# Optimization experiments

Hardware: AMD Instinct MI355X
Metric: run time of the kernel (lower is better)

The kernel has to match this reference:

```python
import jax, jax.numpy as jnp
import numpy as np
from jax import lax

B, S, D = 2, 4096, 1024
E, H, K = 8, 2816, 2  # hidden_dim 4096 -> int(2*4096/3)=2730 -> round up to multiple_of 256 -> 2816


def setup_inputs() -> dict:
    key = jax.random.key(0)
    ks = jax.random.split(key, 5)
    scale = 0.02
    return {
        "x": jax.random.normal(ks[0], (B, S, D), dtype=jnp.float32),
        "router_w": jax.random.normal(ks[1], (E, D), dtype=jnp.float32) * scale,
        "w1": jax.random.normal(ks[2], (E, D, H), dtype=jnp.float32) * scale,
        "w2": jax.random.normal(ks[3], (E, H, D), dtype=jnp.float32) * scale,
        "w3": jax.random.normal(ks[4], (E, D, H), dtype=jnp.float32) * scale,
        "top_k": K,
    }


def reference(x, router_w, w1, w2, w3, top_k):
    b, s, d = x.shape
    e = router_w.shape[0]
    xf = x.reshape(-1, d)                                # [T, D]
    logits = xf @ router_w.T                             # [T, E]
    vals, idx = lax.top_k(logits, top_k)                 # [T, K]
    rw = jax.nn.softmax(vals.astype(jnp.float32), axis=-1).astype(x.dtype)  # [T, K]
    # combine[t, e] = routing weight of expert e for token t (0 if not selected)
    combine = jnp.sum(jax.nn.one_hot(idx, e, dtype=x.dtype) * rw[..., None], axis=1)  # [T, E]

    def body(acc, ew):
        w1e, w2e, w3e, ce = ew                           # [D,H], [H,D], [D,H], [T]
        h = jax.nn.silu(xf @ w1e) * (xf @ w3e)           # SwiGLU FFN, [T, H]
        return acc + (h @ w2e) * ce[:, None], None

    out, _ = lax.scan(body, jnp.zeros_like(xf), (w1, w2, w3, combine.T))
    return out.reshape(b, s, d)
```

## Files before the change

kernel.cpp:

```cpp
#include <hip/hip_runtime.h>
#include <stdint.h>

#define T_TOK 8192
#define DIM   1024
#define NE    8
#define NH    2816
#define NROWS (T_TOK*2)

typedef __attribute__((ext_vector_type(8))) __bf16 bf16x8;
typedef __attribute__((ext_vector_type(4))) float  f32x4;

typedef __attribute__((address_space(1))) const unsigned int g_as1;
typedef __attribute__((address_space(3))) unsigned int l_as3;
#define GLL(g, l) __builtin_amdgcn_global_load_lds((g_as1*)(g), (l_as3*)(l), 16, 0, 0)

__device__ __forceinline__ unsigned short f2bf(float f){
  union { float f; uint32_t u; } v; v.f = f;
  uint32_t r = (v.u + 0x7FFFu + ((v.u >> 16) & 1u)) >> 16;
  return (unsigned short)r;
}


__global__ void init_k(int* counts, int* cursor){
  int i = threadIdx.x;
  if (i < NE){ counts[i] = 0; cursor[i] = 0; }
}

__global__ void zero_out_k(float4* __restrict__ out){
  int i = blockIdx.x*blockDim.x + threadIdx.x;
  const int n4 = T_TOK*DIM/4;
  const float4 z = make_float4(0.f,0.f,0.f,0.f);
  for (; i < n4; i += gridDim.x*blockDim.x) out[i] = z;
}

__global__ void cvt_k(const float* __restrict__ x, unsigned short* __restrict__ xbf){
  int i = blockIdx.x*blockDim.x + threadIdx.x;
  const int total = T_TOK*DIM/8;
  for (; i < total; i += gridDim.x*blockDim.x){
    const float4 a = *(const float4*)(x + (size_t)i*8);
    const float4 b = *(const float4*)(x + (size_t)i*8 + 4);
    ushort4 lo = make_ushort4(f2bf(a.x), f2bf(a.y), f2bf(a.z), f2bf(a.w));
    ushort4 hi = make_ushort4(f2bf(b.x), f2bf(b.y), f2bf(b.z), f2bf(b.w));
    *(ushort4*)(xbf + (size_t)i*8)     = lo;
    *(ushort4*)(xbf + (size_t)i*8 + 4) = hi;
  }
}

__global__ __launch_bounds__(256) void transp_k(const float* __restrict__ in,
    unsigned short* __restrict__ outp, int R, int C)
{
  __shared__ unsigned short Tl[64*68];
  const int r0 = blockIdx.x*64, c0 = blockIdx.y*64;
  const size_t mbase = (size_t)blockIdx.z * (size_t)R * (size_t)C;
  const float* ip = in + mbase;
  unsigned short* op = outp + mbase;
  const int t = threadIdx.x;
  #pragma unroll
  for (int i=0;i<4;i++){
    const int r  = (t>>4) + i*16;
    const int cq = t & 15;
    const float4 v = *(const float4*)(ip + (size_t)(r0+r)*C + c0 + cq*4);
    Tl[(cq*4+0)*68 + r] = f2bf(v.x);
    Tl[(cq*4+1)*68 + r] = f2bf(v.y);
    Tl[(cq*4+2)*68 + r] = f2bf(v.z);
    Tl[(cq*4+3)*68 + r] = f2bf(v.w);
  }
  __syncthreads();
  #pragma unroll
  for (int i=0;i<4;i++){
    const int idx = i*1024 + t*4;
    const int c = idx>>6, r = idx&63;
    const ushort4 v = *(const ushort4*)&Tl[c*68 + r];
    *(ushort4*)(op + (size_t)(c0+c)*R + r0 + r) = v;
  }
}

__global__ __launch_bounds__(256) void transp2_k(const float* __restrict__ w1,
    const float* __restrict__ w3, unsigned short* __restrict__ w1t,
    unsigned short* __restrict__ w3t)
{
  __shared__ unsigned short Tl[64*68];
  const int r0 = blockIdx.x*64, c0 = blockIdx.y*64;
  const int z = blockIdx.z;
  const size_t mbase = (size_t)(z & (NE-1)) * (size_t)DIM * (size_t)NH;
  const float* ip = (z < NE ? w1 : w3) + mbase;
  unsigned short* op = (z < NE ? w1t : w3t) + mbase;
  const int t = threadIdx.x;
  #pragma unroll
  for (int i=0;i<4;i++){
    const int r  = (t>>4) + i*16;
    const int cq = t & 15;
    const float4 v = *(const float4*)(ip + (size_t)(r0+r)*NH + c0 + cq*4);
    Tl[(cq*4+0)*68 + r] = f2bf(v.x);
    Tl[(cq*4+1)*68 + r] = f2bf(v.y);
    Tl[(cq*4+2)*68 + r] = f2bf(v.z);
    Tl[(cq*4+3)*68 + r] = f2bf(v.w);
  }
  __syncthreads();
  #pragma unroll
  for (int i=0;i<4;i++){
    const int idx = i*1024 + t*4;
    const int c = idx>>6, r = idx&63;
    const ushort4 v = *(const ushort4*)&Tl[c*68 + r];
    *(ushort4*)(op + (size_t)(c0+c)*DIM + r0 + r) = v;
  }
}


__global__ void router_k(const float* __restrict__ x, const float* __restrict__ rw,
                         int* __restrict__ topk_e, float* __restrict__ topk_w,
                         int* __restrict__ counts){
  const int t = blockIdx.x;
  const int l = threadIdx.x;
  const float* xr = x + (size_t)t * DIM;
  float acc[NE];
  #pragma unroll
  for (int e=0;e<NE;e++) acc[e] = 0.f;
  #pragma unroll
  for (int i=0;i<DIM/64;i++){
    float xv = xr[l + 64*i];
    #pragma unroll
    for (int e=0;e<NE;e++) acc[e] += xv * rw[e*DIM + l + 64*i];
  }
  #pragma unroll
  for (int e=0;e<NE;e++){
    float v = acc[e];
    #pragma unroll
    for (int off=32; off; off>>=1) v += __shfl_xor(v, off);
    acc[e] = v;
  }
  if (l == 0){
    int e0 = 0; float v0 = acc[0];
    #pragma unroll
    for (int e=1;e<NE;e++) if (acc[e] > v0){ v0 = acc[e]; e0 = e; }
    int e1 = -1; float v1 = -1e30f;
    #pragma unroll
    for (int e=0;e<NE;e++) if (e != e0 && acc[e] > v1){ v1 = acc[e]; e1 = e; }
    float ex = __expf(v1 - v0);
    float s  = 1.f + ex;
    topk_e[t*2]   = e0;  topk_e[t*2+1] = e1;
    topk_w[t*2]   = 1.f/s; topk_w[t*2+1] = ex/s;
    atomicAdd(&counts[e0], 1);
    atomicAdd(&counts[e1], 1);
  }
}

__global__ void prefix_k(const int* __restrict__ counts, int* __restrict__ offs){
  if (threadIdx.x == 0 && blockIdx.x == 0){
    int s = 0;
    for (int e=0;e<NE;e++){ offs[e] = s; s += counts[e]; }
  }
}

__global__ void scatter_k(const int* __restrict__ topk_e, const float* __restrict__ topk_w,
                          const int* __restrict__ offs, int* __restrict__ cursor,
                          int* __restrict__ row_tok, float* __restrict__ row_w){
  int t = blockIdx.x*blockDim.x + threadIdx.x;
  if (t >= T_TOK) return;
  #pragma unroll
  for (int k=0;k<2;k++){
    int e = topk_e[t*2+k];
    int p = atomicAdd(&cursor[e], 1);
    int flat = offs[e] + p;
    row_tok[flat] = t;
    row_w[flat]   = topk_w[t*2+k];
  }
}


__global__ __launch_bounds__(512,2) void gemm1_p(
    const unsigned short* __restrict__ xbf,
    const unsigned short* __restrict__ w1t, const unsigned short* __restrict__ w3t,
    unsigned short* __restrict__ hbuf,
    const int* __restrict__ row_tok,
    const int* __restrict__ counts, const int* __restrict__ offs)
{
  __shared__ unsigned short As [3][128*32];
  __shared__ unsigned short B1s[3][128*32];
  __shared__ unsigned short B3s[3][128*32];

  const int i   = blockIdx.y*64 + blockIdx.x;
  const int lid = (i & 7)*1408 + (i >> 3);
  const int e   = lid / 1408;
  const int rem = lid - e*1408;
  const int h0  = (rem >> 6) * 128;
  const int rb  = rem & 63;

  const int cnt = counts[e];
  const int row0 = rb * 128;
  if (row0 >= cnt) return;
  const int nv   = min(128, cnt - row0);
  const int base = offs[e] + row0;
  const int NK   = DIM/32;

  const int t = threadIdx.x;
  const int r_loc = t >> 2, sct = t & 3;
  const int csw = (sct ^ ((r_loc >> 1) & 3)) * 8;
  const int tok = row_tok[base + min(r_loc, nv-1)];
  const unsigned short* aS  = xbf + (size_t)tok*DIM + csw;
  const unsigned short* b1S = w1t + ((size_t)(e*NH + h0) + r_loc)*DIM + csw;
  const unsigned short* b3S = w3t + ((size_t)(e*NH + h0) + r_loc)*DIM + csw;
  const int lo = t*16;

  const int wid = t >> 6, l = t & 63;
  const int wr = wid >> 2, wc = wid & 3;
  const int lr = l & 15,  lk = l >> 4;
  const int rc = (lk ^ ((lr >> 1) & 3)) * 8;

  f32x4 acc1[4][2], acc3[4][2];
  #pragma unroll
  for (int m=0;m<4;m++)
    #pragma unroll
    for (int n=0;n<2;n++){ acc1[m][n] = (f32x4)0.f; acc3[m][n] = (f32x4)0.f; }

  GLL(aS,      (char*)As[0]+lo); GLL(b1S,      (char*)B1s[0]+lo); GLL(b3S,      (char*)B3s[0]+lo);
  GLL(aS+32,   (char*)As[1]+lo); GLL(b1S+32,   (char*)B1s[1]+lo); GLL(b3S+32,   (char*)B3s[1]+lo);

  for (int kt=0; kt<NK; ++kt){
    if (kt < NK-1) asm volatile("s_waitcnt vmcnt(3)" ::: "memory");
    else           asm volatile("s_waitcnt vmcnt(0)" ::: "memory");
    __builtin_amdgcn_s_barrier();

    if (kt+2 < NK){
      const int kA = (kt+2)*32;
      char* ad  = (char*)As [(kt+2)%3];
      char* b1d = (char*)B1s[(kt+2)%3];
      char* b3d = (char*)B3s[(kt+2)%3];
      GLL(aS+kA, ad+lo); GLL(b1S+kA, b1d+lo); GLL(b3S+kA, b3d+lo);
    }

    const unsigned short* Ab  = As [kt%3];
    const unsigned short* B1b = B1s[kt%3];
    const unsigned short* B3b = B3s[kt%3];

    bf16x8 a[4], b1[2], b3[2];
    #pragma unroll
    for (int m=0;m<4;m++) a[m] = *(const bf16x8*)&Ab[(wr*64 + m*16 + lr)*32 + rc];
    #pragma unroll
    for (int n=0;n<2;n++){
      b1[n] = *(const bf16x8*)&B1b[(wc*32 + n*16 + lr)*32 + rc];
      b3[n] = *(const bf16x8*)&B3b[(wc*32 + n*16 + lr)*32 + rc];
    }
    __builtin_amdgcn_s_setprio(1);
    #pragma unroll
    for (int m=0;m<4;m++)
      #pragma unroll
      for (int n=0;n<2;n++){
        acc1[m][n] = __builtin_amdgcn_mfma_f32_16x16x32_bf16(a[m], b1[n], acc1[m][n], 0,0,0);
        acc3[m][n] = __builtin_amdgcn_mfma_f32_16x16x32_bf16(a[m], b3[n], acc3[m][n], 0,0,0);
      }
    __builtin_amdgcn_s_setprio(0);
  }

  #pragma unroll
  for (int m=0;m<4;m++){
    #pragma unroll
    for (int i2=0;i2<4;i2++){
      const int r = wr*64 + m*16 + lk*4 + i2;
      if (r < nv){
        const size_t rowbase = (size_t)(base + r) * NH;
        #pragma unroll
        for (int n=0;n<2;n++){
          float z  = acc1[m][n][i2];
          float p3 = acc3[m][n][i2];
          float hv = (z / (1.f + __expf(-z))) * p3;
          hbuf[rowbase + h0 + wc*32 + n*16 + lr] = f2bf(hv);
        }
      }
    }
  }
}

__global__ __launch_bounds__(512,2) void gemm2_p(
    const unsigned short* __restrict__ hbuf,
    const unsigned short* __restrict__ w2t,
    float* __restrict__ out,
    const int* __restrict__ row_tok, const float* __restrict__ row_w,
    const int* __restrict__ counts, const int* __restrict__ offs)
{
  __shared__ unsigned short As[3][128*32];
  __shared__ unsigned short Bs[3][128*32];

  const int i   = blockIdx.y*64 + blockIdx.x;
  const int lid = (i & 7)*512 + (i >> 3);
  const int e   = lid >> 9;
  const int rem = lid & 511;
  const int d0  = (rem >> 6) * 128;
  const int rb  = rem & 63;

  const int cnt = counts[e];
  const int row0 = rb * 128;
  if (row0 >= cnt) return;
  const int nv   = min(128, cnt - row0);
  const int base = offs[e] + row0;
  const int NK   = NH/32;

  const int t = threadIdx.x;
  const int r_loc = t >> 2, sct = t & 3;
  const int csw = (sct ^ ((r_loc >> 1) & 3)) * 8;
  const unsigned short* aS = hbuf + (size_t)(base + min(r_loc, nv-1))*NH + csw;
  const unsigned short* bS = w2t + ((size_t)(e*DIM + d0) + r_loc)*NH + csw;
  const int lo = t*16;

  const int wid = t >> 6, l = t & 63;
  const int wr = wid >> 2, wc = wid & 3;
  const int lr = l & 15,  lk = l >> 4;
  const int rc = (lk ^ ((lr >> 1) & 3)) * 8;

  f32x4 acc[4][2];
  #pragma unroll
  for (int m=0;m<4;m++)
    #pragma unroll
    for (int n=0;n<2;n++) acc[m][n] = (f32x4)0.f;

  GLL(aS,    (char*)As[0]+lo); GLL(bS,    (char*)Bs[0]+lo);
  GLL(aS+32, (char*)As[1]+lo); GLL(bS+32, (char*)Bs[1]+lo);

  for (int kt=0; kt<NK; ++kt){
    if (kt < NK-1) asm volatile("s_waitcnt vmcnt(2)" ::: "memory");
    else           asm volatile("s_waitcnt vmcnt(0)" ::: "memory");
    __builtin_amdgcn_s_barrier();

    if (kt+2 < NK){
      const int kA = (kt+2)*32;
      char* ad = (char*)As[(kt+2)%3];
      char* bd = (char*)Bs[(kt+2)%3];
      GLL(aS+kA, ad+lo); GLL(bS+kA, bd+lo);
    }

    const unsigned short* Ab = As[kt%3];
    const unsigned short* Bb = Bs[kt%3];

    bf16x8 a[4], b[2];
    #pragma unroll
    for (int m=0;m<4;m++) a[m] = *(const bf16x8*)&Ab[(wr*64 + m*16 + lr)*32 + rc];
    #pragma unroll
    for (int n=0;n<2;n++)  b[n] = *(const bf16x8*)&Bb[(wc*32 + n*16 + lr)*32 + rc];
    __builtin_amdgcn_s_setprio(1);
    #pragma unroll
    for (int m=0;m<4;m++)
      #pragma unroll
      for (int n=0;n<2;n++)
        acc[m][n] = __builtin_amdgcn_mfma_f32_16x16x32_bf16(a[m], b[n], acc[m][n], 0,0,0);
    __builtin_amdgcn_s_setprio(0);
  }

  #pragma unroll
  for (int m=0;m<4;m++){
    #pragma unroll
    for (int i2=0;i2<4;i2++){
      const int r = wr*64 + m*16 + lk*4 + i2;
      if (r < nv){
        const int flat = base + r;
        const int tok  = row_tok[flat];
        const float wgt = row_w[flat];
        float* orow = out + (size_t)tok * DIM + d0 + wc*32;
        #pragma unroll
        for (int n=0;n<2;n++)
          atomicAdd(&orow[n*16 + lr], acc[m][n][i2] * wgt);
      }
    }
  }
}


__global__ __launch_bounds__(256) void gemm1_k(
    const unsigned short* __restrict__ xbf,
    const float* __restrict__ w1, const float* __restrict__ w3,
    unsigned short* __restrict__ hbuf,
    const int* __restrict__ row_tok,
    const int* __restrict__ counts, const int* __restrict__ offs)
{
  __shared__ unsigned short Al [128*32];
  __shared__ unsigned short B1l[128*32];
  __shared__ unsigned short B3l[128*32];
  const int e   = blockIdx.y >> 6;
  const int rb  = blockIdx.y & 63;
  const int cnt = counts[e];
  const int row0 = rb * 128;
  if (row0 >= cnt) return;
  const int nv   = min(128, cnt - row0);
  const int base = offs[e] + row0;
  const int h0   = blockIdx.x * 128;
  const int t  = threadIdx.x;
  const int ar0 = t >> 2;
  const int ac  = t & 3;
  const int tok0 = row_tok[base + min(ar0,      nv-1)];
  const int tok1 = row_tok[base + min(ar0 + 64, nv-1)];
  const size_t asrc0 = (size_t)tok0 * DIM + ac*8;
  const size_t asrc1 = (size_t)tok1 * DIM + ac*8;
  const int dg = t >> 5;
  const int hq = t & 31;
  const float* w1p = w1 + (size_t)e * DIM * NH + (size_t)(h0 + hq*4);
  const float* w3p = w3 + (size_t)e * DIM * NH + (size_t)(h0 + hq*4);
  const int wid = t >> 6, l = t & 63;
  const int wr = wid >> 1, wc = wid & 1;
  const int lr = l & 15,  lk = l >> 4;
  f32x4 acc1[4][4], acc3[4][4];
  #pragma unroll
  for (int m=0;m<4;m++)
    #pragma unroll
    for (int n=0;n<4;n++){ acc1[m][n] = (f32x4)0.f; acc3[m][n] = (f32x4)0.f; }
  for (int kk=0; kk<DIM/32; ++kk){
    const int k0 = kk*32;
    __syncthreads();
    *(uint4*)&Al[ar0*32 + ac*8]      = *(const uint4*)(xbf + asrc0 + k0);
    *(uint4*)&Al[(ar0+64)*32 + ac*8] = *(const uint4*)(xbf + asrc1 + k0);
    {
      const float4 f0 = *(const float4*)(w1p + (size_t)(k0 + dg*4 + 0)*NH);
      const float4 f1 = *(const float4*)(w1p + (size_t)(k0 + dg*4 + 1)*NH);
      const float4 f2 = *(const float4*)(w1p + (size_t)(k0 + dg*4 + 2)*NH);
      const float4 f3 = *(const float4*)(w1p + (size_t)(k0 + dg*4 + 3)*NH);
      const float* p0=(const float*)&f0; const float* p1=(const float*)&f1;
      const float* p2=(const float*)&f2; const float* p3=(const float*)&f3;
      #pragma unroll
      for (int j=0;j<4;j++){
        ushort4 pk = make_ushort4(f2bf(p0[j]), f2bf(p1[j]), f2bf(p2[j]), f2bf(p3[j]));
        *(ushort4*)&B1l[(hq*4+j)*32 + dg*4] = pk;
      }
      const float4 g0 = *(const float4*)(w3p + (size_t)(k0 + dg*4 + 0)*NH);
      const float4 g1 = *(const float4*)(w3p + (size_t)(k0 + dg*4 + 1)*NH);
      const float4 g2 = *(const float4*)(w3p + (size_t)(k0 + dg*4 + 2)*NH);
      const float4 g3 = *(const float4*)(w3p + (size_t)(k0 + dg*4 + 3)*NH);
      const float* q0=(const float*)&g0; const float* q1=(const float*)&g1;
      const float* q2=(const float*)&g2; const float* q3=(const float*)&g3;
      #pragma unroll
      for (int j=0;j<4;j++){
        ushort4 pk = make_ushort4(f2bf(q0[j]), f2bf(q1[j]), f2bf(q2[j]), f2bf(q3[j]));
        *(ushort4*)&B3l[(hq*4+j)*32 + dg*4] = pk;
      }
    }
    __syncthreads();
    bf16x8 a[4], b1[4], b3[4];
    #pragma unroll
    for (int m=0;m<4;m++) a[m] = *(const bf16x8*)&Al[(wr*64 + m*16 + lr)*32 + lk*8];
    #pragma unroll
    for (int n=0;n<4;n++){
      b1[n] = *(const bf16x8*)&B1l[(wc*64 + n*16 + lr)*32 + lk*8];
      b3[n] = *(const bf16x8*)&B3l[(wc*64 + n*16 + lr)*32 + lk*8];
    }
    #pragma unroll
    for (int m=0;m<4;m++)
      #pragma unroll
      for (int n=0;n<4;n++){
        acc1[m][n] = __builtin_amdgcn_mfma_f32_16x16x32_bf16(a[m], b1[n], acc1[m][n], 0,0,0);
        acc3[m][n] = __builtin_amdgcn_mfma_f32_16x16x32_bf16(a[m], b3[n], acc3[m][n], 0,0,0);
      }
  }
  #pragma unroll
  for (int m=0;m<4;m++){
    #pragma unroll
    for (int i=0;i<4;i++){
      const int r = wr*64 + m*16 + lk*4 + i;
      if (r < nv){
        const size_t rowbase = (size_t)(base + r) * NH;
        #pragma unroll
        for (int n=0;n<4;n++){
          float z  = acc1[m][n][i];
          float p3 = acc3[m][n][i];
          float hv = (z / (1.f + __expf(-z))) * p3;
          hbuf[rowbase + h0 + wc*64 + n*16 + lr] = f2bf(hv);
        }
      }
    }
  }
}

__global__ __launch_bounds__(256) void gemm2_k(
    const unsigned short* __restrict__ hbuf,
    const float* __restrict__ w2,
    float* __restrict__ out,
    const int* __restrict__ row_tok, const float* __restrict__ row_w,
    const int* __restrict__ counts, const int* __restrict__ offs)
{
  __shared__ unsigned short Al[128*32];
  __shared__ unsigned short Bl[128*32];
  const int e   = blockIdx.y >> 6;
  const int rb  = blockIdx.y & 63;
  const int cnt = counts[e];
  const int row0 = rb * 128;
  if (row0 >= cnt) return;
  const int nv   = min(128, cnt - row0);
  const int base = offs[e] + row0;
  const int d0   = blockIdx.x * 128;
  const int t  = threadIdx.x;
  const int ar0 = t >> 2;
  const int ac  = t & 3;
  const size_t asrc0 = (size_t)(base + min(ar0,      nv-1)) * NH + ac*8;
  const size_t asrc1 = (size_t)(base + min(ar0 + 64, nv-1)) * NH + ac*8;
  const int dg = t >> 5;
  const int hq = t & 31;
  const float* w2p = w2 + (size_t)e * NH * DIM + (size_t)(d0 + hq*4);
  const int wid = t >> 6, l = t & 63;
  const int wr = wid >> 1, wc = wid & 1;
  const int lr = l & 15,  lk = l >> 4;
  f32x4 acc[4][4];
  #pragma unroll
  for (int m=0;m<4;m++)
    #pragma unroll
    for (int n=0;n<4;n++) acc[m][n] = (f32x4)0.f;
  for (int kk=0; kk<NH/32; ++kk){
    const int k0 = kk*32;
    __syncthreads();
    *(uint4*)&Al[ar0*32 + ac*8]      = *(const uint4*)(hbuf + asrc0 + k0);
    *(uint4*)&Al[(ar0+64)*32 + ac*8] = *(const uint4*)(hbuf + asrc1 + k0);
    {
      const float4 f0 = *(const float4*)(w2p + (size_t)(k0 + dg*4 + 0)*DIM);
      const float4 f1 = *(const float4*)(w2p + (size_t)(k0 + dg*4 + 1)*DIM);
      const float4 f2 = *(const float4*)(w2p + (size_t)(k0 + dg*4 + 2)*DIM);
      const float4 f3 = *(const float4*)(w2p + (size_t)(k0 + dg*4 + 3)*DIM);
      const float* p0=(const float*)&f0; const float* p1=(const float*)&f1;
      const float* p2=(const float*)&f2; const float* p3=(const float*)&f3;
      #pragma unroll
      for (int j=0;j<4;j++){
        ushort4 pk = make_ushort4(f2bf(p0[j]), f2bf(p1[j]), f2bf(p2[j]), f2bf(p3[j]));
        *(ushort4*)&Bl[(hq*4+j)*32 + dg*4] = pk;
      }
    }
    __syncthreads();
    bf16x8 a[4], b[4];
    #pragma unroll
    for (int m=0;m<4;m++) a[m] = *(const bf16x8*)&Al[(wr*64 + m*16 + lr)*32 + lk*8];
    #pragma unroll
    for (int n=0;n<4;n++)  b[n] = *(const bf16x8*)&Bl[(wc*64 + n*16 + lr)*32 + lk*8];
    #pragma unroll
    for (int m=0;m<4;m++)
      #pragma unroll
      for (int n=0;n<4;n++)
        acc[m][n] = __builtin_amdgcn_mfma_f32_16x16x32_bf16(a[m], b[n], acc[m][n], 0,0,0);
  }
  #pragma unroll
  for (int m=0;m<4;m++){
    #pragma unroll
    for (int i=0;i<4;i++){
      const int r = wr*64 + m*16 + lk*4 + i;
      if (r < nv){
        const int flat = base + r;
        const int tok  = row_tok[flat];
        const float wgt = row_w[flat];
        float* orow = out + (size_t)tok * DIM + d0 + wc*64;
        #pragma unroll
        for (int n=0;n<4;n++)
          atomicAdd(&orow[n*16 + lr], acc[m][n][i] * wgt);
      }
    }
  }
}


extern "C" void kernel_launch(void* const* d_in, const int* in_sizes, int n_in,
                              void* d_out, int out_size, void* d_ws, size_t ws_size,
                              hipStream_t stream) {
  (void)in_sizes; (void)n_in; (void)out_size;
  const float* x   = (const float*)d_in[0];
  const float* rw  = (const float*)d_in[1];
  const float* w1  = (const float*)d_in[2];
  const float* w2  = (const float*)d_in[3];
  const float* w3  = (const float*)d_in[4];
  float* out = (float*)d_out;
  char* ws = (char*)d_ws;

  const size_t SZ_XBF  = (size_t)T_TOK*DIM*2;
  const size_t SZ_HBUF = (size_t)NROWS*NH*2;
  const size_t SZ_WT   = (size_t)NE*NH*DIM*2;
  const size_t SZ_SMALL = (size_t)NROWS*4*2 + (size_t)T_TOK*2*4*2 + 3*64*4 + 4096;
  const size_t NEED_FAST = SZ_XBF + SZ_HBUF + 2*SZ_WT + SZ_SMALL;

  if (ws_size >= NEED_FAST) {
    size_t off = 0;
    unsigned short* xbf  = (unsigned short*)(ws + off); off += SZ_XBF;
    unsigned short* hbuf = (unsigned short*)(ws + off); off += SZ_HBUF;
    unsigned short* w1t  = (unsigned short*)(ws + off); off += SZ_WT;
    unsigned short* w3t  = (unsigned short*)(ws + off); off += SZ_WT;
    unsigned short* w2t  = w1t;
    int*   row_tok = (int*)  (ws + off); off += NROWS*4;
    float* row_w   = (float*)(ws + off); off += NROWS*4;
    int*   topk_e  = (int*)  (ws + off); off += T_TOK*2*4;
    float* topk_w  = (float*)(ws + off); off += T_TOK*2*4;
    int*   counts  = (int*)  (ws + off); off += 64;
    int*   offs    = (int*)  (ws + off); off += 64;
    int*   cursor  = (int*)  (ws + off); off += 64;

    init_k    <<<1, 64, 0, stream>>>(counts, cursor);
    zero_out_k<<<2048, 256, 0, stream>>>((float4*)out);
    cvt_k     <<<2048, 256, 0, stream>>>(x, xbf);
    router_k  <<<T_TOK, 64, 0, stream>>>(x, rw, topk_e, topk_w, counts);
    prefix_k  <<<1, 64, 0, stream>>>(counts, offs);
    scatter_k <<<(T_TOK+255)/256, 256, 0, stream>>>(topk_e, topk_w, offs, cursor, row_tok, row_w);
    transp2_k <<<dim3(DIM/64, NH/64, 2*NE), 256, 0, stream>>>(w1, w3, w1t, w3t);
    gemm1_p   <<<dim3(64, NE*22), 512, 0, stream>>>(xbf, w1t, w3t, hbuf, row_tok, counts, offs);
    transp_k  <<<dim3(NH/64, DIM/64, NE), 256, 0, stream>>>(w2, w2t, NH, DIM);
    gemm2_p   <<<dim3(64, NE*8), 512, 0, stream>>>(hbuf, w2t, out, row_tok, row_w, counts, offs);
  } else {
    size_t off = 0;
    unsigned short* xbf  = (unsigned short*)(ws + off); off += SZ_XBF;
    unsigned short* hbuf = (unsigned short*)(ws + off); off += SZ_HBUF;
    int*   row_tok = (int*)  (ws + off); off += NROWS*4;
    float* row_w   = (float*)(ws + off); off += NROWS*4;
    int*   topk_e  = (int*)  (ws + off); off += T_TOK*2*4;
    float* topk_w  = (float*)(ws + off); off += T_TOK*2*4;
    int*   counts  = (int*)  (ws + off); off += 64;
    int*   offs    = (int*)  (ws + off); off += 64;
    int*   cursor  = (int*)  (ws + off); off += 64;

    init_k    <<<1, 64, 0, stream>>>(counts, cursor);
    zero_out_k<<<2048, 256, 0, stream>>>((float4*)out);
    cvt_k     <<<2048, 256, 0, stream>>>(x, xbf);
    router_k  <<<T_TOK, 64, 0, stream>>>(x, rw, topk_e, topk_w, counts);
    prefix_k  <<<1, 64, 0, stream>>>(counts, offs);
    scatter_k <<<(T_TOK+255)/256, 256, 0, stream>>>(topk_e, topk_w, offs, cursor, row_tok, row_w);
    gemm1_k   <<<dim3(NH/128, NE*64), 256, 0, stream>>>(xbf, w1, w3, hbuf, row_tok, counts, offs);
    gemm2_k   <<<dim3(DIM/128, NE*64), 256, 0, stream>>>(hbuf, w2, out, row_tok, row_w, counts, offs);
  }
}
```

Before: 755.9 us.

## Enlarge grouped GEMM tiles to 256 rows/cols with double-buffered LDS

gemm1 now handles 256 token rows per block (8 M-fragments per wave) and gemm2 handles 256 output columns per block (4 N-fragments per wave). The aim is more reuse of each weight and activation tile loaded into LDS and fewer blocks. To fit the larger tiles, the pipeline drops from three LDS buffers to two, and a second barrier per k-step guards buffer reuse. This raises register pressure, since gemm1 keeps 32 accumulators per wave, and it reduces the distance of load/compute overlap.

```diff
diff --git a/kernel.cpp b/kernel.cpp
--- a/kernel.cpp
+++ b/kernel.cpp
@@ -13,6 +13,7 @@
 typedef __attribute__((address_space(1))) const unsigned int g_as1;
 typedef __attribute__((address_space(3))) unsigned int l_as3;
 #define GLL(g, l) __builtin_amdgcn_global_load_lds((g_as1*)(g), (l_as3*)(l), 16, 0, 0)
+#define MFMA16(a,b,c) __builtin_amdgcn_mfma_f32_16x16x32_bf16(a,b,c,0,0,0)
 
 __device__ __forceinline__ unsigned short f2bf(float f){
   union { float f; uint32_t u; } v; v.f = f;
@@ -168,16 +169,16 @@
 }
 
 
-__global__ __launch_bounds__(512,2) void gemm1_p(
+__global__ __launch_bounds__(512,2) void gemm1_q(
     const unsigned short* __restrict__ xbf,
     const unsigned short* __restrict__ w1t, const unsigned short* __restrict__ w3t,
     unsigned short* __restrict__ hbuf,
     const int* __restrict__ row_tok,
     const int* __restrict__ counts, const int* __restrict__ offs)
 {
-  __shared__ unsigned short As [3][128*32];
-  __shared__ unsigned short B1s[3][128*32];
-  __shared__ unsigned short B3s[3][128*32];
+  __shared__ unsigned short As [2][256*32];
+  __shared__ unsigned short B1s[2][128*32];
+  __shared__ unsigned short B3s[2][128*32];
 
   const int i   = blockIdx.y*64 + blockIdx.x;
   const int lid = (i & 7)*1408 + (i >> 3);
@@ -186,18 +187,20 @@
   const int h0  = (rem >> 6) * 128;
   const int rb  = rem & 63;
 
-  const int cnt = counts[e];
-  const int row0 = rb * 128;
+  const int cnt  = counts[e];
+  const int row0 = rb * 256;
   if (row0 >= cnt) return;
-  const int nv   = min(128, cnt - row0);
+  const int nv   = min(256, cnt - row0);
   const int base = offs[e] + row0;
   const int NK   = DIM/32;
 
   const int t = threadIdx.x;
   const int r_loc = t >> 2, sct = t & 3;
   const int csw = (sct ^ ((r_loc >> 1) & 3)) * 8;
-  const int tok = row_tok[base + min(r_loc, nv-1)];
-  const unsigned short* aS  = xbf + (size_t)tok*DIM + csw;
+  const int tokA = row_tok[base + min(r_loc,       nv-1)];
+  const int tokB = row_tok[base + min(r_loc + 128, nv-1)];
+  const unsigned short* aP0 = xbf + (size_t)tokA*DIM + csw;
+  const unsigned short* aP1 = xbf + (size_t)tokB*DIM + csw;
   const unsigned short* b1S = w1t + ((size_t)(e*NH + h0) + r_loc)*DIM + csw;
   const unsigned short* b3S = w3t + ((size_t)(e*NH + h0) + r_loc)*DIM + csw;
   const int lo = t*16;
@@ -205,58 +208,62 @@
   const int wid = t >> 6, l = t & 63;
   const int wr = wid >> 2, wc = wid & 3;
   const int lr = l & 15,  lk = l >> 4;
-  const int rc = (lk ^ ((lr >> 1) & 3)) * 8;
-
-  f32x4 acc1[4][2], acc3[4][2];
-  #pragma unroll
-  for (int m=0;m<4;m++)
+
+  f32x4 acc1[8][2], acc3[8][2];
+  #pragma unroll
+  for (int m=0;m<8;m++)
     #pragma unroll
     for (int n=0;n<2;n++){ acc1[m][n] = (f32x4)0.f; acc3[m][n] = (f32x4)0.f; }
 
-  GLL(aS,      (char*)As[0]+lo); GLL(b1S,      (char*)B1s[0]+lo); GLL(b3S,      (char*)B3s[0]+lo);
-  GLL(aS+32,   (char*)As[1]+lo); GLL(b1S+32,   (char*)B1s[1]+lo); GLL(b3S+32,   (char*)B3s[1]+lo);
+  GLL(aP0, (char*)As[0] + lo); GLL(aP1, (char*)As[0] + 8192 + lo);
+  GLL(b1S, (char*)B1s[0] + lo); GLL(b3S, (char*)B3s[0] + lo);
 
   for (int kt=0; kt<NK; ++kt){
-    if (kt < NK-1) asm volatile("s_waitcnt vmcnt(3)" ::: "memory");
-    else           asm volatile("s_waitcnt vmcnt(0)" ::: "memory");
+    const int cur = kt & 1;
+    if (kt+1 < NK){
+      const int k1 = (kt+1)*32;
+      GLL(aP0+k1, (char*)As[cur^1] + lo); GLL(aP1+k1, (char*)As[cur^1] + 8192 + lo);
+      GLL(b1S+k1, (char*)B1s[cur^1] + lo); GLL(b3S+k1, (char*)B3s[cur^1] + lo);
+      asm volatile("s_waitcnt vmcnt(4)" ::: "memory");
+    } else {
+      asm volatile("s_waitcnt vmcnt(0)" ::: "memory");
+    }
     __builtin_amdgcn_s_barrier();
 
-    if (kt+2 < NK){
-      const int kA = (kt+2)*32;
-      char* ad  = (char*)As [(kt+2)%3];
-      char* b1d = (char*)B1s[(kt+2)%3];
-      char* b3d = (char*)B3s[(kt+2)%3];
-      GLL(aS+kA, ad+lo); GLL(b1S+kA, b1d+lo); GLL(b3S+kA, b3d+lo);
-    }
-
-    const unsigned short* Ab  = As [kt%3];
-    const unsigned short* B1b = B1s[kt%3];
-    const unsigned short* B3b = B3s[kt%3];
-
-    bf16x8 a[4], b1[2], b3[2];
-    #pragma unroll
-    for (int m=0;m<4;m++) a[m] = *(const bf16x8*)&Ab[(wr*64 + m*16 + lr)*32 + rc];
+    const unsigned short* Ab  = As [cur];
+    const unsigned short* B1b = B1s[cur];
+    const unsigned short* B3b = B3s[cur];
+
+    bf16x8 a[8], b1[2], b3[2];
+    #pragma unroll
+    for (int m=0;m<8;m++){
+      const int row = wr*128 + m*16 + lr;
+      a[m] = *(const bf16x8*)&Ab[row*32 + ((lk ^ ((row>>1)&3))<<3)];
+    }
     #pragma unroll
     for (int n=0;n<2;n++){
-      b1[n] = *(const bf16x8*)&B1b[(wc*32 + n*16 + lr)*32 + rc];
-      b3[n] = *(const bf16x8*)&B3b[(wc*32 + n*16 + lr)*32 + rc];
+      const int row = wc*32 + n*16 + lr;
+      const int off = row*32 + ((lk ^ ((row>>1)&3))<<3);
+      b1[n] = *(const bf16x8*)&B1b[off];
+      b3[n] = *(const bf16x8*)&B3b[off];
     }
     __builtin_amdgcn_s_setprio(1);
     #pragma unroll
-    for (int m=0;m<4;m++)
+    for (int m=0;m<8;m++)
       #pragma unroll
       for (int n=0;n<2;n++){
-        acc1[m][n] = __builtin_amdgcn_mfma_f32_16x16x32_bf16(a[m], b1[n], acc1[m][n], 0,0,0);
-        acc3[m][n] = __builtin_amdgcn_mfma_f32_16x16x32_bf16(a[m], b3[n], acc3[m][n], 0,0,0);
+        acc1[m][n] = MFMA16(a[m], b1[n], acc1[m][n]);
+        acc3[m][n] = MFMA16(a[m], b3[n], acc3[m][n]);
       }
     __builtin_amdgcn_s_setprio(0);
-  }
-
-  #pragma unroll
-  for (int m=0;m<4;m++){
+    __builtin_amdgcn_s_barrier();
+  }
+
+  #pragma unroll
+  for (int m=0;m<8;m++){
     #pragma unroll
     for (int i2=0;i2<4;i2++){
-      const int r = wr*64 + m*16 + lk*4 + i2;
+      const int r = wr*128 + m*16 + lk*4 + i2;
       if (r < nv){
         const size_t rowbase = (size_t)(base + r) * NH;
         #pragma unroll
@@ -271,24 +278,24 @@
   }
 }
 
-__global__ __launch_bounds__(512,2) void gemm2_p(
+__global__ __launch_bounds__(512,2) void gemm2_q(
     const unsigned short* __restrict__ hbuf,
     const unsigned short* __restrict__ w2t,
     float* __restrict__ out,
     const int* __restrict__ row_tok, const float* __restrict__ row_w,
     const int* __restrict__ counts, const int* __restrict__ offs)
 {
-  __shared__ unsigned short As[3][128*32];
-  __shared__ unsigned short Bs[3][128*32];
+  __shared__ unsigned short As[2][128*32];
+  __shared__ unsigned short Bs[2][256*32];
 
   const int i   = blockIdx.y*64 + blockIdx.x;
-  const int lid = (i & 7)*512 + (i >> 3);
-  const int e   = lid >> 9;
-  const int rem = lid & 511;
-  const int d0  = (rem >> 6) * 128;
+  const int lid = (i & 7)*256 + (i >> 3);
+  const int e   = lid >> 8;
+  const int rem = lid & 255;
+  const int d0  = (rem >> 6) * 256;
   const int rb  = rem & 63;
 
-  const int cnt = counts[e];
+  const int cnt  = counts[e];
   const int row0 = rb * 128;
   if (row0 >= cnt) return;
   const int nv   = min(128, cnt - row0);
@@ -298,51 +305,58 @@
   const int t = threadIdx.x;
   const int r_loc = t >> 2, sct = t & 3;
   const int csw = (sct ^ ((r_loc >> 1) & 3)) * 8;
-  const unsigned short* aS = hbuf + (size_t)(base + min(r_loc, nv-1))*NH + csw;
-  const unsigned short* bS = w2t + ((size_t)(e*DIM + d0) + r_loc)*NH + csw;
+  const unsigned short* aS  = hbuf + (size_t)(base + min(r_loc, nv-1))*NH + csw;
+  const unsigned short* bS0 = w2t + ((size_t)(e*DIM + d0) + r_loc)*NH + csw;
+  const unsigned short* bS1 = bS0 + (size_t)128*NH;
   const int lo = t*16;
 
   const int wid = t >> 6, l = t & 63;
   const int wr = wid >> 2, wc = wid & 3;
   const int lr = l & 15,  lk = l >> 4;
-  const int rc = (lk ^ ((lr >> 1) & 3)) * 8;
-
-  f32x4 acc[4][2];
+
+  f32x4 acc[4][4];
   #pragma unroll
   for (int m=0;m<4;m++)
     #pragma unroll
-    for (int n=0;n<2;n++) acc[m][n] = (f32x4)0.f;
-
-  GLL(aS,    (char*)As[0]+lo); GLL(bS,    (char*)Bs[0]+lo);
-  GLL(aS+32, (char*)As[1]+lo); GLL(bS+32, (char*)Bs[1]+lo);
+    for (int n=0;n<4;n++) acc[m][n] = (f32x4)0.f;
+
+  GLL(aS,  (char*)As[0] + lo);
+  GLL(bS0, (char*)Bs[0] + lo); GLL(bS1, (char*)Bs[0] + 8192 + lo);
 
   for (int kt=0; kt<NK; ++kt){
-    if (kt < NK-1) asm volatile("s_waitcnt vmcnt(2)" ::: "memory");
-    else           asm volatile("s_waitcnt vmcnt(0)" ::: "memory");
+    const int cur = kt & 1;
+    if (kt+1 < NK){
+      const int k1 = (kt+1)*32;
+      GLL(aS+k1,  (char*)As[cur^1] + lo);
+      GLL(bS0+k1, (char*)Bs[cur^1] + lo); GLL(bS1+k1, (char*)Bs[cur^1] + 8192 + lo);
+      asm volatile("s_waitcnt vmcnt(3)" ::: "memory");
+    } else {
+      asm volatile("s_waitcnt vmcnt(0)" ::: "memory");
+    }
     __builtin_amdgcn_s_barrier();
 
-    if (kt+2 < NK){
-      const int kA = (kt+2)*32;
-      char* ad = (char*)As[(kt+2)%3];
-      char* bd = (char*)Bs[(kt+2)%3];
-      GLL(aS+kA, ad+lo); GLL(bS+kA, bd+lo);
-    }
-
-    const unsigned short* Ab = As[kt%3];
-    const unsigned short* Bb = Bs[kt%3];
-
-    bf16x8 a[4], b[2];
-    #pragma unroll
-    for (int m=0;m<4;m++) a[m] = *(const bf16x8*)&Ab[(wr*64 + m*16 + lr)*32 + rc];
-    #pragma unroll
-    for (int n=0;n<2;n++)  b[n] = *(const bf16x8*)&Bb[(wc*32 + n*16 + lr)*32 + rc];
+    const unsigned short* Ab = As[cur];
+    const unsigned short* Bb = Bs[cur];
+
+    bf16x8 a[4], b[4];
+    #pragma unroll
+    for (int m=0;m<4;m++){
+      const int row = wr*64 + m*16 + lr;
+      a[m] = *(const bf16x8*)&Ab[row*32 + ((lk ^ ((row>>1)&3))<<3)];
+    }
+    #pragma unroll
+    for (int n=0;n<4;n++){
+      const int row = wc*64 + n*16 + lr;
+      b[n] = *(const bf16x8*)&Bb[row*32 + ((lk ^ ((row>>1)&3))<<3)];
+    }
     __builtin_amdgcn_s_setprio(1);
     #pragma unroll
     for (int m=0;m<4;m++)
       #pragma unroll
-      for (int n=0;n<2;n++)
-        acc[m][n] = __builtin_amdgcn_mfma_f32_16x16x32_bf16(a[m], b[n], acc[m][n], 0,0,0);
+      for (int n=0;n<4;n++)
+        acc[m][n] = MFMA16(a[m], b[n], acc[m][n]);
     __builtin_amdgcn_s_setprio(0);
+    __builtin_amdgcn_s_barrier();
   }
 
   #pragma unroll
@@ -354,9 +368,9 @@
         const int flat = base + r;
         const int tok  = row_tok[flat];
         const float wgt = row_w[flat];
-        float* orow = out + (size_t)tok * DIM + d0 + wc*32;
+        float* orow = out + (size_t)tok * DIM + d0 + wc*64;
         #pragma unroll
-        for (int n=0;n<2;n++)
+        for (int n=0;n<4;n++)
           atomicAdd(&orow[n*16 + lr], acc[m][n][i2] * wgt);
       }
     }
@@ -443,8 +457,8 @@
     for (int m=0;m<4;m++)
       #pragma unroll
       for (int n=0;n<4;n++){
-        acc1[m][n] = __builtin_amdgcn_mfma_f32_16x16x32_bf16(a[m], b1[n], acc1[m][n], 0,0,0);
-        acc3[m][n] = __builtin_amdgcn_mfma_f32_16x16x32_bf16(a[m], b3[n], acc3[m][n], 0,0,0);
+        acc1[m][n] = MFMA16(a[m], b1[n], acc1[m][n]);
+        acc3[m][n] = MFMA16(a[m], b3[n], acc3[m][n]);
       }
   }
   #pragma unroll
@@ -527,7 +541,7 @@
     for (int m=0;m<4;m++)
       #pragma unroll
       for (int n=0;n<4;n++)
-        acc[m][n] = __builtin_amdgcn_mfma_f32_16x16x32_bf16(a[m], b[n], acc[m][n], 0,0,0);
+        acc[m][n] = MFMA16(a[m], b[n], acc[m][n]);
   }
   #pragma unroll
   for (int m=0;m<4;m++){
@@ -588,9 +602,9 @@
     prefix_k  <<<1, 64, 0, stream>>>(counts, offs);
     scatter_k <<<(T_TOK+255)/256, 256, 0, stream>>>(topk_e, topk_w, offs, cursor, row_tok, row_w);
     transp2_k <<<dim3(DIM/64, NH/64, 2*NE), 256, 0, stream>>>(w1, w3, w1t, w3t);
-    gemm1_p   <<<dim3(64, NE*22), 512, 0, stream>>>(xbf, w1t, w3t, hbuf, row_tok, counts, offs);
+    gemm1_q   <<<dim3(64, 176), 512, 0, stream>>>(xbf, w1t, w3t, hbuf, row_tok, counts, offs);
     transp_k  <<<dim3(NH/64, DIM/64, NE), 256, 0, stream>>>(w2, w2t, NH, DIM);
-    gemm2_p   <<<dim3(64, NE*8), 512, 0, stream>>>(hbuf, w2t, out, row_tok, row_w, counts, offs);
+    gemm2_q   <<<dim3(64, 32), 512, 0, stream>>>(hbuf, w2t, out, row_tok, row_w, counts, offs);
   } else {
     size_t off = 0;
     unsigned short* xbf  = (unsigned short*)(ws + off); off += SZ_XBF;
```

Measured after the change: 891.6 us. +18.0%, slower.

## Fuse setup kernels and merge weight transposes into one launch

Applied to the files above, without the earlier changes.

Folds the counter initialization into the output-zeroing kernel and the x-to-bf16 conversion into the router kernel, removing two launches and a second read of x. All three weight transposes go into one kernel with wider 16-byte stores and a padded LDS stride. When the workspace is large enough, w2 gets its own buffer so every transpose runs before gemm1 instead of in between the GEMMs. This needs more workspace, and the router now does vectorized float4 loads.

```diff
diff --git a/kernel.cpp b/kernel.cpp
--- a/kernel.cpp
+++ b/kernel.cpp
@@ -9,10 +9,12 @@
 
 typedef __attribute__((ext_vector_type(8))) __bf16 bf16x8;
 typedef __attribute__((ext_vector_type(4))) float  f32x4;
+typedef __attribute__((ext_vector_type(8))) unsigned short ushort8;
 
 typedef __attribute__((address_space(1))) const unsigned int g_as1;
 typedef __attribute__((address_space(3))) unsigned int l_as3;
 #define GLL(g, l) __builtin_amdgcn_global_load_lds((g_as1*)(g), (l_as3*)(l), 16, 0, 0)
+#define MFMA16(a,b,c) __builtin_amdgcn_mfma_f32_16x16x32_bf16(a,b,c,0,0,0)
 
 __device__ __forceinline__ unsigned short f2bf(float f){
   union { float f; uint32_t u; } v; v.f = f;
@@ -21,12 +23,8 @@
 }
 
 
-__global__ void init_k(int* counts, int* cursor){
-  int i = threadIdx.x;
-  if (i < NE){ counts[i] = 0; cursor[i] = 0; }
-}
-
-__global__ void zero_out_k(float4* __restrict__ out){
+__global__ void zero_init_k(float4* __restrict__ out, int* counts, int* cursor){
+  if (blockIdx.x == 0 && threadIdx.x < NE){ counts[threadIdx.x] = 0; cursor[threadIdx.x] = 0; }
   int i = blockIdx.x*blockDim.x + threadIdx.x;
   const int n4 = T_TOK*DIM/4;
   const float4 z = make_float4(0.f,0.f,0.f,0.f);
@@ -46,81 +44,74 @@
   }
 }
 
-__global__ __launch_bounds__(256) void transp_k(const float* __restrict__ in,
-    unsigned short* __restrict__ outp, int R, int C)
+
+__global__ __launch_bounds__(256) void transpA_k(
+    const float* __restrict__ w1, const float* __restrict__ w3,
+    const float* __restrict__ w2,
+    unsigned short* __restrict__ w1t, unsigned short* __restrict__ w3t,
+    unsigned short* __restrict__ w2t, int zbase)
 {
-  __shared__ unsigned short Tl[64*68];
-  const int r0 = blockIdx.x*64, c0 = blockIdx.y*64;
-  const size_t mbase = (size_t)blockIdx.z * (size_t)R * (size_t)C;
-  const float* ip = in + mbase;
-  unsigned short* op = outp + mbase;
+  __shared__ unsigned short Tl[64*72];
+  const int z = zbase + blockIdx.y;
+  const int f = blockIdx.x;
+  const size_t DS = (size_t)DIM*NH;
+  const float* src; unsigned short* dst; int R, C, rt, ct;
+  if (z < 16){
+    R = DIM; C = NH; rt = f/44; ct = f - rt*44;
+    const int e = z & 7;
+    src = (z < 8 ? w1 : w3) + (size_t)e*DS;
+    dst = (z < 8 ? w1t : w3t) + (size_t)e*DS;
+  } else {
+    R = NH; C = DIM; rt = f/16; ct = f - rt*16;
+    const int e = z - 16;
+    src = w2 + (size_t)e*DS;
+    dst = w2t + (size_t)e*DS;
+  }
+  const int r0 = rt*64, c0 = ct*64;
   const int t = threadIdx.x;
   #pragma unroll
   for (int i=0;i<4;i++){
     const int r  = (t>>4) + i*16;
     const int cq = t & 15;
-    const float4 v = *(const float4*)(ip + (size_t)(r0+r)*C + c0 + cq*4);
-    Tl[(cq*4+0)*68 + r] = f2bf(v.x);
-    Tl[(cq*4+1)*68 + r] = f2bf(v.y);
-    Tl[(cq*4+2)*68 + r] = f2bf(v.z);
-    Tl[(cq*4+3)*68 + r] = f2bf(v.w);
+    const float4 v = *(const float4*)(src + (size_t)(r0+r)*C + c0 + cq*4);
+    Tl[(cq*4+0)*72 + r] = f2bf(v.x);
+    Tl[(cq*4+1)*72 + r] = f2bf(v.y);
+    Tl[(cq*4+2)*72 + r] = f2bf(v.z);
+    Tl[(cq*4+3)*72 + r] = f2bf(v.w);
   }
   __syncthreads();
   #pragma unroll
-  for (int i=0;i<4;i++){
-    const int idx = i*1024 + t*4;
-    const int c = idx>>6, r = idx&63;
-    const ushort4 v = *(const ushort4*)&Tl[c*68 + r];
-    *(ushort4*)(op + (size_t)(c0+c)*R + r0 + r) = v;
-  }
-}
-
-__global__ __launch_bounds__(256) void transp2_k(const float* __restrict__ w1,
-    const float* __restrict__ w3, unsigned short* __restrict__ w1t,
-    unsigned short* __restrict__ w3t)
-{
-  __shared__ unsigned short Tl[64*68];
-  const int r0 = blockIdx.x*64, c0 = blockIdx.y*64;
-  const int z = blockIdx.z;
-  const size_t mbase = (size_t)(z & (NE-1)) * (size_t)DIM * (size_t)NH;
-  const float* ip = (z < NE ? w1 : w3) + mbase;
-  unsigned short* op = (z < NE ? w1t : w3t) + mbase;
-  const int t = threadIdx.x;
-  #pragma unroll
-  for (int i=0;i<4;i++){
-    const int r  = (t>>4) + i*16;
-    const int cq = t & 15;
-    const float4 v = *(const float4*)(ip + (size_t)(r0+r)*NH + c0 + cq*4);
-    Tl[(cq*4+0)*68 + r] = f2bf(v.x);
-    Tl[(cq*4+1)*68 + r] = f2bf(v.y);
-    Tl[(cq*4+2)*68 + r] = f2bf(v.z);
-    Tl[(cq*4+3)*68 + r] = f2bf(v.w);
-  }
-  __syncthreads();
-  #pragma unroll
-  for (int i=0;i<4;i++){
-    const int idx = i*1024 + t*4;
-    const int c = idx>>6, r = idx&63;
-    const ushort4 v = *(const ushort4*)&Tl[c*68 + r];
-    *(ushort4*)(op + (size_t)(c0+c)*DIM + r0 + r) = v;
+  for (int i=0;i<2;i++){
+    const int c  = i*32 + (t>>3);
+    const int r8 = (t&7)*8;
+    const ushort8 v = *(const ushort8*)&Tl[c*72 + r8];
+    *(ushort8*)(dst + (size_t)(c0+c)*R + r0 + r8) = v;
   }
 }
 
 
 __global__ void router_k(const float* __restrict__ x, const float* __restrict__ rw,
+                         unsigned short* __restrict__ xbf,
                          int* __restrict__ topk_e, float* __restrict__ topk_w,
                          int* __restrict__ counts){
   const int t = blockIdx.x;
   const int l = threadIdx.x;
   const float* xr = x + (size_t)t * DIM;
+  unsigned short* xo = xbf + (size_t)t * DIM;
   float acc[NE];
   #pragma unroll
   for (int e=0;e<NE;e++) acc[e] = 0.f;
   #pragma unroll
-  for (int i=0;i<DIM/64;i++){
-    float xv = xr[l + 64*i];
-    #pragma unroll
-    for (int e=0;e<NE;e++) acc[e] += xv * rw[e*DIM + l + 64*i];
+  for (int i=0;i<4;i++){
+    const int idx = l*4 + i*256;
+    const float4 xv = *(const float4*)(xr + idx);
+    ushort4 pk = make_ushort4(f2bf(xv.x), f2bf(xv.y), f2bf(xv.z), f2bf(xv.w));
+    *(ushort4*)(xo + idx) = pk;
+    #pragma unroll
+    for (int e=0;e<NE;e++){
+      const float4 wv = *(const float4*)(rw + e*DIM + idx);
+      acc[e] += xv.x*wv.x + xv.y*wv.y + xv.z*wv.z + xv.w*wv.w;
+    }
   }
   #pragma unroll
   for (int e=0;e<NE;e++){
@@ -213,8 +204,8 @@
     #pragma unroll
     for (int n=0;n<2;n++){ acc1[m][n] = (f32x4)0.f; acc3[m][n] = (f32x4)0.f; }
 
-  GLL(aS,      (char*)As[0]+lo); GLL(b1S,      (char*)B1s[0]+lo); GLL(b3S,      (char*)B3s[0]+lo);
-  GLL(aS+32,   (char*)As[1]+lo); GLL(b1S+32,   (char*)B1s[1]+lo); GLL(b3S+32,   (char*)B3s[1]+lo);
+  GLL(aS,    (char*)As[0]+lo); GLL(b1S,    (char*)B1s[0]+lo); GLL(b3S,    (char*)B3s[0]+lo);
+  GLL(aS+32, (char*)As[1]+lo); GLL(b1S+32, (char*)B1s[1]+lo); GLL(b3S+32, (char*)B3s[1]+lo);
 
   for (int kt=0; kt<NK; ++kt){
     if (kt < NK-1) asm volatile("s_waitcnt vmcnt(3)" ::: "memory");
@@ -246,8 +237,8 @@
     for (int m=0;m<4;m++)
       #pragma unroll
       for (int n=0;n<2;n++){
-        acc1[m][n] = __builtin_amdgcn_mfma_f32_16x16x32_bf16(a[m], b1[n], acc1[m][n], 0,0,0);
-        acc3[m][n] = __builtin_amdgcn_mfma_f32_16x16x32_bf16(a[m], b3[n], acc3[m][n], 0,0,0);
+        acc1[m][n] = MFMA16(a[m], b1[n], acc1[m][n]);
+        acc3[m][n] = MFMA16(a[m], b3[n], acc3[m][n]);
       }
     __builtin_amdgcn_s_setprio(0);
   }
@@ -341,7 +332,7 @@
     for (int m=0;m<4;m++)
       #pragma unroll
       for (int n=0;n<2;n++)
-        acc[m][n] = __builtin_amdgcn_mfma_f32_16x16x32_bf16(a[m], b[n], acc[m][n], 0,0,0);
+        acc[m][n] = MFMA16(a[m], b[n], acc[m][n]);
     __builtin_amdgcn_s_setprio(0);
   }
 
@@ -443,8 +434,8 @@
     for (int m=0;m<4;m++)
       #pragma unroll
       for (int n=0;n<4;n++){
-        acc1[m][n] = __builtin_amdgcn_mfma_f32_16x16x32_bf16(a[m], b1[n], acc1[m][n], 0,0,0);
-        acc3[m][n] = __builtin_amdgcn_mfma_f32_16x16x32_bf16(a[m], b3[n], acc3[m][n], 0,0,0);
+        acc1[m][n] = MFMA16(a[m], b1[n], acc1[m][n]);
+        acc3[m][n] = MFMA16(a[m], b3[n], acc3[m][n]);
       }
   }
   #pragma unroll
@@ -527,7 +518,7 @@
     for (int m=0;m<4;m++)
       #pragma unroll
       for (int n=0;n<4;n++)
-        acc[m][n] = __builtin_amdgcn_mfma_f32_16x16x32_bf16(a[m], b[n], acc[m][n], 0,0,0);
+        acc[m][n] = MFMA16(a[m], b[n], acc[m][n]);
   }
   #pragma unroll
   for (int m=0;m<4;m++){
@@ -565,14 +556,18 @@
   const size_t SZ_WT   = (size_t)NE*NH*DIM*2;
   const size_t SZ_SMALL = (size_t)NROWS*4*2 + (size_t)T_TOK*2*4*2 + 3*64*4 + 4096;
   const size_t NEED_FAST = SZ_XBF + SZ_HBUF + 2*SZ_WT + SZ_SMALL;
+  const size_t NEED_FULL = SZ_XBF + SZ_HBUF + 3*SZ_WT + SZ_SMALL;
 
   if (ws_size >= NEED_FAST) {
+    const bool full = (ws_size >= NEED_FULL);
     size_t off = 0;
     unsigned short* xbf  = (unsigned short*)(ws + off); off += SZ_XBF;
     unsigned short* hbuf = (unsigned short*)(ws + off); off += SZ_HBUF;
     unsigned short* w1t  = (unsigned short*)(ws + off); off += SZ_WT;
     unsigned short* w3t  = (unsigned short*)(ws + off); off += SZ_WT;
-    unsigned short* w2t  = w1t;
+    unsigned short* w2t;
+    if (full){ w2t = (unsigned short*)(ws + off); off += SZ_WT; }
+    else      { w2t = w1t; }
     int*   row_tok = (int*)  (ws + off); off += NROWS*4;
     float* row_w   = (float*)(ws + off); off += NROWS*4;
     int*   topk_e  = (int*)  (ws + off); off += T_TOK*2*4;
@@ -581,16 +576,20 @@
     int*   offs    = (int*)  (ws + off); off += 64;
     int*   cursor  = (int*)  (ws + off); off += 64;
 
-    init_k    <<<1, 64, 0, stream>>>(counts, cursor);
-    zero_out_k<<<2048, 256, 0, stream>>>((float4*)out);
-    cvt_k     <<<2048, 256, 0, stream>>>(x, xbf);
-    router_k  <<<T_TOK, 64, 0, stream>>>(x, rw, topk_e, topk_w, counts);
-    prefix_k  <<<1, 64, 0, stream>>>(counts, offs);
-    scatter_k <<<(T_TOK+255)/256, 256, 0, stream>>>(topk_e, topk_w, offs, cursor, row_tok, row_w);
-    transp2_k <<<dim3(DIM/64, NH/64, 2*NE), 256, 0, stream>>>(w1, w3, w1t, w3t);
-    gemm1_p   <<<dim3(64, NE*22), 512, 0, stream>>>(xbf, w1t, w3t, hbuf, row_tok, counts, offs);
-    transp_k  <<<dim3(NH/64, DIM/64, NE), 256, 0, stream>>>(w2, w2t, NH, DIM);
-    gemm2_p   <<<dim3(64, NE*8), 512, 0, stream>>>(hbuf, w2t, out, row_tok, row_w, counts, offs);
+    zero_init_k<<<2048, 256, 0, stream>>>((float4*)out, counts, cursor);
+    router_k   <<<T_TOK, 64, 0, stream>>>(x, rw, xbf, topk_e, topk_w, counts);
+    prefix_k   <<<1, 64, 0, stream>>>(counts, offs);
+    scatter_k  <<<(T_TOK+255)/256, 256, 0, stream>>>(topk_e, topk_w, offs, cursor, row_tok, row_w);
+    if (full){
+      transpA_k <<<dim3(704, 24), 256, 0, stream>>>(w1, w3, w2, w1t, w3t, w2t, 0);
+      gemm1_p   <<<dim3(64, 176), 512, 0, stream>>>(xbf, w1t, w3t, hbuf, row_tok, counts, offs);
+      gemm2_p   <<<dim3(64, NE*8), 512, 0, stream>>>(hbuf, w2t, out, row_tok, row_w, counts, offs);
+    } else {
+      transpA_k <<<dim3(704, 16), 256, 0, stream>>>(w1, w3, w2, w1t, w3t, w2t, 0);
+      gemm1_p   <<<dim3(64, 176), 512, 0, stream>>>(xbf, w1t, w3t, hbuf, row_tok, counts, offs);
+      transpA_k <<<dim3(704, 8), 256, 0, stream>>>(w1, w3, w2, w1t, w3t, w2t, 16);
+      gemm2_p   <<<dim3(64, NE*8), 512, 0, stream>>>(hbuf, w2t, out, row_tok, row_w, counts, offs);
+    }
   } else {
     size_t off = 0;
     unsigned short* xbf  = (unsigned short*)(ws + off); off += SZ_XBF;
@@ -603,13 +602,11 @@
     int*   offs    = (int*)  (ws + off); off += 64;
     int*   cursor  = (int*)  (ws + off); off += 64;
 
-    init_k    <<<1, 64, 0, stream>>>(counts, cursor);
-    zero_out_k<<<2048, 256, 0, stream>>>((float4*)out);
-    cvt_k     <<<2048, 256, 0, stream>>>(x, xbf);
-    router_k  <<<T_TOK, 64, 0, stream>>>(x, rw, topk_e, topk_w, counts);
-    prefix_k  <<<1, 64, 0, stream>>>(counts, offs);
-    scatter_k <<<(T_TOK+255)/256, 256, 0, stream>>>(topk_e, topk_w, offs, cursor, row_tok, row_w);
-    gemm1_k   <<<dim3(NH/128, NE*64), 256, 0, stream>>>(xbf, w1, w3, hbuf, row_tok, counts, offs);
-    gemm2_k   <<<dim3(DIM/128, NE*64), 256, 0, stream>>>(hbuf, w2, out, row_tok, row_w, counts, offs);
-  }
-}
+    zero_init_k<<<2048, 256, 0, stream>>>((float4*)out, counts, cursor);
+    router_k   <<<T_TOK, 64, 0, stream>>>(x, rw, xbf, topk_e, topk_w, counts);
+    prefix_k   <<<1, 64, 0, stream>>>(counts, offs);
+    scatter_k  <<<(T_TOK+255)/256, 256, 0, stream>>>(topk_e, topk_w, offs, cursor, row_tok, row_w);
+    gemm1_k    <<<dim3(NH/128, NE*64), 256, 0, stream>>>(xbf, w1, w3, hbuf, row_tok, counts, offs);
+    gemm2_k    <<<dim3(DIM/128, NE*64), 256, 0, stream>>>(hbuf, w2, out, row_tok, row_w, counts, offs);
+  }
+}
```

After: 751.4 us. Within noise of the previous version (-0.6%).
